# Performance work log

Measured on AMD Instinct MI355X. Metric: run time of the kernel, lower is better.

## Reference

```python
import jax, jax.numpy as jnp
import numpy as np

N, TX, NH, H, E, V = 64, 1024, 512, 512, 300, 32000
IP = NH + H            # attention input size = 1024
HALF = IP // 2         # 512
BN_EPS = 1e-5


def setup_inputs() -> dict:
    key = jax.random.key(0)
    ks = jax.random.split(key, 24)
    p = lambda k, shape: jax.random.normal(k, shape, dtype=jnp.float32) * 0.05
    embed_W = p(ks[0], (V, E)).at[0].set(0.0)  # padding_idx=0 row zeroed
    return {
        "yt_prev": jax.random.randint(ks[1], (N,), 0, V, dtype=jnp.int32),
        "h0": jax.random.normal(ks[2], (N, H), dtype=jnp.float32),
        "c0": jax.random.normal(ks[3], (N, H), dtype=jnp.float32),
        "h1": jax.random.normal(ks[4], (N, H), dtype=jnp.float32),
        "c1": jax.random.normal(ks[5], (N, H), dtype=jnp.float32),
        "encoder_output": jax.random.normal(ks[6], (N, TX, NH), dtype=jnp.float32),
        "c_prev": jax.random.normal(ks[7], (N, NH), dtype=jnp.float32),
        "embed_W": embed_W,
        # pre LSTM cell: input = NH + E
        "pre_W_ih": p(ks[8], (4 * H, NH + E)), "pre_W_hh": p(ks[9], (4 * H, H)),
        "pre_b_ih": p(ks[10], (4 * H,)), "pre_b_hh": p(ks[11], (4 * H,)),
        # post LSTM cell: input = H + NH
        "post_W_ih": p(ks[12], (4 * H, H + NH)), "post_W_hh": p(ks[13], (4 * H, H)),
        "post_b_ih": p(ks[14], (4 * H,)), "post_b_hh": p(ks[15], (4 * H,)),
        # attention MLP
        "att_W1": p(ks[16], (HALF, IP)), "att_b1": p(ks[17], (HALF,)),
        "att_W2": p(ks[18], (1, HALF)), "att_b2": p(ks[19], (1,)),
        # classifier
        "mlp_W": p(ks[20], (V, H)), "mlp_b": p(ks[21], (V,)),
        "bn_gamma": jnp.ones((V,), jnp.float32), "bn_beta": jnp.zeros((V,), jnp.float32),
    }


def _lstm_cell(x, h, c, W_ih, W_hh, b_ih, b_hh):
    # PyTorch LSTMCell gate order: i, f, g, o
    g = x @ W_ih.T + h @ W_hh.T + (b_ih + b_hh)
    i, f, gg, o = jnp.split(g, 4, axis=-1)
    c_new = jax.nn.sigmoid(f) * c + jax.nn.sigmoid(i) * jnp.tanh(gg)
    h_new = jax.nn.sigmoid(o) * jnp.tanh(c_new)
    return h_new, c_new


def reference(yt_prev, h0, c0, h1, c1, encoder_output, c_prev, embed_W,
              pre_W_ih, pre_W_hh, pre_b_ih, pre_b_hh,
              post_W_ih, post_W_hh, post_b_ih, post_b_hh,
              att_W1, att_b1, att_W2, att_b2,
              mlp_W, mlp_b, bn_gamma, bn_beta):
    # embedding lookup + concat with previous context
    y_emb = embed_W[yt_prev]                              # [N, E]
    rnn_input = jnp.concatenate([y_emb, c_prev], axis=1)  # [N, E+NH]
    h_0, c_0 = _lstm_cell(rnn_input, h0, c0, pre_W_ih, pre_W_hh, pre_b_ih, pre_b_hh)
    s_i = h_0
    # Bahdanau attention over encoder timesteps
    Tx = encoder_output.shape[1]
    s_exp = jnp.broadcast_to(s_i[:, None, :], (s_i.shape[0], Tx, s_i.shape[1]))
    concat = jnp.concatenate([encoder_output, s_exp], axis=2)  # [N, Tx, IP]
    e = jax.nn.relu(concat @ att_W1.T + att_b1)                # [N, Tx, HALF]
    scores = e @ att_W2.T + att_b2                             # [N, Tx, 1]
    alphas = jax.nn.softmax(scores, axis=1)                    # softmax over Tx
    context = jnp.sum(alphas * encoder_output, axis=1)         # [N, NH]
    # post LSTM cell
    spell_input = jnp.concatenate([s_i, context], axis=1)
    h_1, c_1 = _lstm_cell(spell_input, h1, c1, post_W_ih, post_W_hh, post_b_ih, post_b_hh)
    # classifier: linear -> relu -> batchnorm(train mode, batch stats) -> softmax
    z = jax.nn.relu(h_1 @ mlp_W.T + mlp_b)                     # [N, V]
    mean = jnp.mean(z, axis=0)
    var = jnp.mean((z - mean) ** 2, axis=0)                    # biased, as in PyTorch training
    z_bn = bn_gamma * (z - mean) * jax.lax.rsqrt(var + BN_EPS) + bn_beta
    out = jax.nn.softmax(z_bn, axis=1)
    return out, h_0, c_0, h_1, c_1, context
```

## Files before the change

### kernel.cpp

```cpp
#include <hip/hip_runtime.h>
#include <math.h>

#define DEVFN __device__ __forceinline__

typedef __attribute__((ext_vector_type(4))) float f32x4;
typedef __attribute__((ext_vector_type(8))) __bf16 bf16x8;
typedef __attribute__((ext_vector_type(4))) short short4v;
typedef __attribute__((ext_vector_type(8))) short short8v;

#define NB   64
#define TXD  1024
#define NHD  512
#define HSZ  512
#define ESZ  300
#define VSZ  32000
#define G4   (4*HSZ)
#define KPRE (ESZ + NHD + HSZ)
#define KPOST 1536
#define HALFD 512

DEVFN short f2bf(float f) {
  unsigned u = __float_as_uint(f);
  u = (u + 0x7fffu + ((u >> 16) & 1u)) >> 16;
  return (short)u;
}
DEVFN float sigm(float x) { return 1.0f / (1.0f + __expf(-x)); }

DEVFN short8v pack8(float4 a, float4 b) {
  short8v v;
  v[0]=f2bf(a.x); v[1]=f2bf(a.y); v[2]=f2bf(a.z); v[3]=f2bf(a.w);
  v[4]=f2bf(b.x); v[5]=f2bf(b.y); v[6]=f2bf(b.z); v[7]=f2bf(b.w);
  return v;
}
DEVFN short4v pack4(float4 a) {
  short4v v;
  v[0]=f2bf(a.x); v[1]=f2bf(a.y); v[2]=f2bf(a.z); v[3]=f2bf(a.w);
  return v;
}
DEVFN void gload16(const void* g, void* lds_base) {
  __builtin_amdgcn_global_load_lds(
      (const __attribute__((address_space(1))) unsigned int*)g,
      (__attribute__((address_space(3))) unsigned int*)lds_base, 16, 0, 0);
}

DEVFN float4 ldA4(const float* __restrict__ A, int lda, int row, int k, int Ka) {
  if (k >= Ka) { float4 z = {0.f,0.f,0.f,0.f}; return z; }
  return *(const float4*)(A + (size_t)row * lda + k);
}
DEVFN float4 ldB4(const float* __restrict__ B1, int ldb1, int split,
                  const float* __restrict__ B2, int ldb2, int row, int k, int Ka) {
  if (k >= Ka) { float4 z = {0.f,0.f,0.f,0.f}; return z; }
  if (k < split) return *(const float4*)(B1 + (size_t)row * ldb1 + k);
  return *(const float4*)(B2 + (size_t)row * ldb2 + (k - split));
}

__global__ __launch_bounds__(256)
void prep(const int* __restrict__ yt, const float* __restrict__ embW,
          const float* __restrict__ c_prev, const float* __restrict__ h0,
          const float* __restrict__ W1, unsigned short* __restrict__ W1b,
          float* __restrict__ cat)
{
  int b = blockIdx.x;
  if (b < 128) {
    int i = b * 256 + threadIdx.x;
    int c = i >> 6, kq = (i & 63) * 8;
    float4 a = *(const float4*)(W1 + (size_t)c * 1024 + kq);
    float4 bb = *(const float4*)(W1 + (size_t)c * 1024 + kq + 4);
    *(short8v*)(W1b + (size_t)c * 512 + kq) = pack8(a, bb);
  } else {
    int i = (b - 128) * 256 + threadIdx.x;
    if (i >= NB * KPRE) return;
    int n = i / KPRE, c = i - n * KPRE;
    float v;
    if (c < ESZ)            v = embW[(size_t)yt[n] * ESZ + c];
    else if (c < ESZ + NHD) v = c_prev[(size_t)n * NHD + (c - ESZ)];
    else                    v = h0[(size_t)n * HSZ + (c - ESZ - NHD)];
    cat[i] = v;
  }
}

template<int EPI>
__global__ __launch_bounds__(256)
void mfma_gemm128(const float* __restrict__ A, int lda, int Ka,
                  const float* __restrict__ B1, int ldb1, int split,
                  const float* __restrict__ B2, int ldb2,
                  const float* __restrict__ bias1,
                  float* __restrict__ C, int ldc, int Kslice,
                  const float* __restrict__ gamma, const float* __restrict__ beta,
                  float* __restrict__ bnsc, float* __restrict__ bnsh)
{
  __shared__ __align__(16) short As[64][40];
  __shared__ __align__(16) short Bs[128][40];
  const int tid = threadIdx.x;
  const int w = tid >> 6, lane = tid & 63;
  const int wr = w >> 1, wc = w & 1;
  const int cl = lane & 15, g = lane >> 4;
  const int n0 = blockIdx.x * 128;
  const int ks = blockIdx.y;
  const int kbeg = ks * Kslice;
  const int kend = min(kbeg + Kslice, Ka);
  C += (size_t)ks * 64 * ldc;

  const f32x4 fz = {0.f,0.f,0.f,0.f};
  f32x4 acc[2][4];
  #pragma unroll
  for (int i = 0; i < 2; ++i)
    #pragma unroll
    for (int j = 0; j < 4; ++j) acc[i][j] = fz;

  const int sr  = tid >> 2;
  const int skc = (tid & 3) * 8;

  float4 ra0, ra1, rb0[2], rb1[2];
  ra0 = ldA4(A, lda, sr, kbeg + skc, Ka);
  ra1 = ldA4(A, lda, sr, kbeg + skc + 4, Ka);
  #pragma unroll
  for (int it = 0; it < 2; ++it) {
    rb0[it] = ldB4(B1, ldb1, split, B2, ldb2, n0 + sr + it*64, kbeg + skc, Ka);
    rb1[it] = ldB4(B1, ldb1, split, B2, ldb2, n0 + sr + it*64, kbeg + skc + 4, Ka);
  }

  for (int k0 = kbeg; k0 < kend; k0 += 32) {
    __syncthreads();
    *(short8v*)&As[sr][skc] = pack8(ra0, ra1);
    #pragma unroll
    for (int it = 0; it < 2; ++it)
      *(short8v*)&Bs[sr + it*64][skc] = pack8(rb0[it], rb1[it]);
    __syncthreads();
    if (k0 + 32 < kend) {
      ra0 = ldA4(A, lda, sr, k0 + 32 + skc, Ka);
      ra1 = ldA4(A, lda, sr, k0 + 32 + skc + 4, Ka);
      #pragma unroll
      for (int it = 0; it < 2; ++it) {
        rb0[it] = ldB4(B1, ldb1, split, B2, ldb2, n0 + sr + it*64, k0 + 32 + skc, Ka);
        rb1[it] = ldB4(B1, ldb1, split, B2, ldb2, n0 + sr + it*64, k0 + 32 + skc + 4, Ka);
      }
    }
    bf16x8 af[2], bfr[4];
    #pragma unroll
    for (int mi = 0; mi < 2; ++mi)
      af[mi] = *(const bf16x8*)&As[wr*32 + mi*16 + cl][g * 8];
    #pragma unroll
    for (int ni = 0; ni < 4; ++ni)
      bfr[ni] = *(const bf16x8*)&Bs[wc*64 + ni*16 + cl][g * 8];
    #pragma unroll
    for (int mi = 0; mi < 2; ++mi)
      #pragma unroll
      for (int ni = 0; ni < 4; ++ni)
        acc[mi][ni] = __builtin_amdgcn_mfma_f32_16x16x32_bf16(af[mi], bfr[ni], acc[mi][ni], 0, 0, 0);
  }

  float s1[4] = {0.f,0.f,0.f,0.f}, s2[4] = {0.f,0.f,0.f,0.f};
  #pragma unroll
  for (int ni = 0; ni < 4; ++ni) {
    int nn = n0 + wc*64 + ni*16 + cl;
    float b = (EPI == 4) ? bias1[nn] : 0.f;
    #pragma unroll
    for (int mi = 0; mi < 2; ++mi)
      #pragma unroll
      for (int r = 0; r < 4; ++r) {
        int m = wr*32 + mi*16 + g*4 + r;
        float v = acc[mi][ni][r];
        if (EPI == 4) v = fmaxf(v + b, 0.f);
        C[(size_t)m * ldc + nn] = v;
        if (EPI == 4) { s1[ni] += v; s2[ni] = fmaf(v, v, s2[ni]); }
      }
  }
  if (EPI == 4) {
    #pragma unroll
    for (int mm = 16; mm < 64; mm <<= 1)
      #pragma unroll
      for (int ni = 0; ni < 4; ++ni) {
        s1[ni] += __shfl_xor(s1[ni], mm, 64);
        s2[ni] += __shfl_xor(s2[ni], mm, 64);
      }
    float* red = (float*)As;
    __syncthreads();
    if (g == 0) {
      #pragma unroll
      for (int ni = 0; ni < 4; ++ni) {
        int col = wc*64 + ni*16 + cl;
        red[(wr*128 + col)*2 + 0] = s1[ni];
        red[(wr*128 + col)*2 + 1] = s2[ni];
      }
    }
    __syncthreads();
    if (tid < 128) {
      int col = n0 + tid;
      float a1 = red[tid*2] + red[(128 + tid)*2];
      float a2 = red[tid*2 + 1] + red[(128 + tid)*2 + 1];
      float mean = a1 * (1.0f / NB);
      float var = a2 * (1.0f / NB) - mean * mean;
      float rr = rsqrtf(var + 1e-5f);
      float sc = gamma[col] * rr;
      bnsc[col] = sc;
      bnsh[col] = beta[col] - mean * sc;
    }
  }
}

__global__ __launch_bounds__(256)
void lstm_point2(const float* __restrict__ gp, int np,
                 const float* __restrict__ bih, const float* __restrict__ bhh,
                 const float* __restrict__ c_old,
                 float* __restrict__ h_new, float* __restrict__ c_new)
{
  int i = blockIdx.x * 256 + threadIdx.x;
  int n = i >> 9, k = i & 511;
  float g[4];
  #pragma unroll
  for (int j = 0; j < 4; ++j) {
    int idx = j * 512 + k;
    float s = bih[idx] + bhh[idx];
    for (int ks = 0; ks < np; ++ks)
      s += gp[((size_t)ks*64 + n) * G4 + idx];
    g[j] = s;
  }
  float c = sigm(g[1]) * c_old[i] + sigm(g[0]) * tanhf(g[2]);
  float h = sigm(g[3]) * tanhf(c);
  h_new[i] = h; c_new[i] = c;
}

__global__ __launch_bounds__(512)
void att_fused(const float* __restrict__ enc, const unsigned short* __restrict__ W1b,
               const float* __restrict__ W2, const float* __restrict__ sprojp,
               const float* __restrict__ b1,
               float* __restrict__ mbuf, float* __restrict__ sbuf,
               float* __restrict__ ctxp)
{
  __shared__ __align__(16) char Asmem[2 * 4096];
  __shared__ float red[512];
  __shared__ float eV[64];
  __shared__ __align__(16) f32x4 red4[512];
  const int tid = threadIdx.x;
  const int wid = tid >> 6, lane = tid & 63;
  const int cl = lane & 15, g = lane >> 4;
  const int r0 = blockIdx.x << 6;
  const int n  = blockIdx.x >> 4;
  const int c0 = wid << 6;

  const int a_row = tid >> 3, a_q = tid & 7;
  const int a_waddr = (a_row >> 1)*128 + (a_row & 1)*64
                    + (((a_q >> 1) ^ ((a_row >> 1) & 3)) << 4) + (a_q & 1)*8;
  const float* a_src = enc + (size_t)(r0 + a_row) * 512 + a_q * 4;
  const unsigned short* bp0 = W1b + (size_t)(c0 + cl) * 512 + g * 8;

  const f32x4 fz = {0.f,0.f,0.f,0.f};
  f32x4 acc[4][4];
  #pragma unroll
  for (int mi = 0; mi < 4; ++mi)
    #pragma unroll
    for (int ni = 0; ni < 4; ++ni) acc[mi][ni] = fz;

  float4 av;
  bf16x8 bcur[4], bnext[4];
  av = *(const float4*)(a_src);
  #pragma unroll
  for (int ni = 0; ni < 4; ++ni)
    bcur[ni] = *(const bf16x8*)(bp0 + ni * 8192);
  *(short4v*)(Asmem + a_waddr) = pack4(av);
  av = *(const float4*)(a_src + 32);
  asm volatile("s_waitcnt lgkmcnt(0)" ::: "memory");
  __builtin_amdgcn_s_barrier();
  __builtin_amdgcn_sched_barrier(0);

  for (int t = 0; t < 16; ++t) {
    const int s = t & 1;
    if (t < 15) {
      *(short4v*)(Asmem + (s ^ 1) * 4096 + a_waddr) = pack4(av);
      #pragma unroll
      for (int ni = 0; ni < 4; ++ni)
        bnext[ni] = *(const bf16x8*)(bp0 + ni * 8192 + (t + 1) * 32);
    }
    if (t < 14) av = *(const float4*)(a_src + (t + 2) * 32);
    const char* Ab = Asmem + s * 4096;
    bf16x8 af[4];
    #pragma unroll
    for (int mi = 0; mi < 4; ++mi) {
      int r = mi * 16 + cl;
      af[mi] = *(const bf16x8*)(Ab + (r >> 1) * 128 + (r & 1) * 64
                                + ((g ^ ((r >> 1) & 3)) << 4));
    }
    #pragma unroll
    for (int mi = 0; mi < 4; ++mi)
      #pragma unroll
      for (int ni = 0; ni < 4; ++ni)
        acc[mi][ni] = __builtin_amdgcn_mfma_f32_16x16x32_bf16(af[mi], bcur[ni], acc[mi][ni], 0, 0, 0);
    if (t < 15) {
      #pragma unroll
      for (int ni = 0; ni < 4; ++ni) bcur[ni] = bnext[ni];
      asm volatile("s_waitcnt lgkmcnt(0)" ::: "memory");
      __builtin_amdgcn_s_barrier();
      __builtin_amdgcn_sched_barrier(0);
    }
  }
  __syncthreads();

  float part[4][4] = {};
  #pragma unroll
  for (int ni = 0; ni < 4; ++ni) {
    int c = c0 + ni*16 + cl;
    float spv = b1[c];
    #pragma unroll
    for (int ks = 0; ks < 4; ++ks)
      spv += sprojp[((size_t)ks*64 + n) * HALFD + c];
    float w2 = W2[c];
    #pragma unroll
    for (int mi = 0; mi < 4; ++mi)
      #pragma unroll
      for (int r = 0; r < 4; ++r)
        part[mi][r] += fmaxf(acc[mi][ni][r] + spv, 0.f) * w2;
  }
  #pragma unroll
  for (int mm = 1; mm < 16; mm <<= 1)
    #pragma unroll
    for (int mi = 0; mi < 4; ++mi)
      #pragma unroll
      for (int r = 0; r < 4; ++r)
        part[mi][r] += __shfl_xor(part[mi][r], mm, 64);
  if (cl == 0) {
    #pragma unroll
    for (int mi = 0; mi < 4; ++mi)
      #pragma unroll
      for (int r = 0; r < 4; ++r)
        red[wid*64 + mi*16 + g*4 + r] = part[mi][r];
  }
  __syncthreads();
  if (tid < 64) {
    float s = 0.f;
    #pragma unroll
    for (int w = 0; w < 8; ++w) s += red[w*64 + tid];
    float M = s;
    #pragma unroll
    for (int mm = 32; mm >= 1; mm >>= 1) M = fmaxf(M, __shfl_xor(M, mm, 64));
    float e = __expf(s - M);
    eV[tid] = e;
    float S = e;
    #pragma unroll
    for (int mm = 32; mm >= 1; mm >>= 1) S += __shfl_xor(S, mm, 64);
    if (tid == 0) { mbuf[blockIdx.x] = M; sbuf[blockIdx.x] = S; }
  }
  __syncthreads();

  {
    const int cgrp = tid & 127, tq = tid >> 7;
    const float* ebase = enc + (size_t)r0 * 512 + (cgrp << 2);
    f32x4 a4 = fz;
    #pragma unroll 8
    for (int tt = 0; tt < 16; ++tt) {
      int t = tq*16 + tt;
      float et = eV[t];
      float4 x = *(const float4*)(ebase + (size_t)t * 512);
      a4[0] = fmaf(et, x.x, a4[0]);
      a4[1] = fmaf(et, x.y, a4[1]);
      a4[2] = fmaf(et, x.z, a4[2]);
      a4[3] = fmaf(et, x.w, a4[3]);
    }
    red4[tq*128 + cgrp] = a4;
  }
  __syncthreads();
  if (tid < 128) {
    f32x4 s4 = red4[tid];
    f32x4 b4 = red4[128 + tid];
    f32x4 c4 = red4[256 + tid];
    f32x4 d4 = red4[384 + tid];
    f32x4 o4;
    #pragma unroll
    for (int i = 0; i < 4; ++i) o4[i] = s4[i] + b4[i] + c4[i] + d4[i];
    *(f32x4*)(ctxp + (size_t)blockIdx.x * 512 + tid*4) = o4;
  }
}

__global__ __launch_bounds__(256)
void att_combine(const float* __restrict__ mbuf, const float* __restrict__ sbuf,
                 const float* __restrict__ ctxp, const float* __restrict__ h0out,
                 const float* __restrict__ h1in,
                 float* __restrict__ ctx_out, float* __restrict__ cat)
{
  int i = blockIdx.x * 256 + threadIdx.x;
  int n = i >> 9, c = i & 511;
  float M = -1e30f;
  #pragma unroll
  for (int b = 0; b < 16; ++b) M = fmaxf(M, mbuf[n*16 + b]);
  float S = 0.f, ctx = 0.f;
  #pragma unroll
  for (int b = 0; b < 16; ++b) {
    float w = __expf(mbuf[n*16 + b] - M);
    S = fmaf(sbuf[n*16 + b], w, S);
    ctx = fmaf(ctxp[(size_t)(n*16 + b)*512 + c], w, ctx);
  }
  ctx /= S;
  ctx_out[i] = ctx;
  cat[(size_t)n * KPOST + c] = h0out[i];
  cat[(size_t)n * KPOST + HSZ + c] = ctx;
  cat[(size_t)n * KPOST + 2*HSZ + c] = h1in[i];
}

__global__ __launch_bounds__(1024)
void softmax_v(const float* __restrict__ z, const float* __restrict__ scale,
               const float* __restrict__ shift, float* __restrict__ out)
{
  int n = blockIdx.x, tid = threadIdx.x;
  const float* zr = z + (size_t)n * VSZ;
  float* orow = out + (size_t)n * VSZ;
  __shared__ float rb[16];
  __shared__ float sb[16];
  float v[32]; float mx = -1e30f;
  #pragma unroll
  for (int i = 0; i < 32; ++i) {
    int j = tid + i*1024;
    v[i] = (j < VSZ) ? fmaf(zr[j], scale[j], shift[j]) : -1e30f;
    mx = fmaxf(mx, v[i]);
  }
  #pragma unroll
  for (int m = 32; m >= 1; m >>= 1) mx = fmaxf(mx, __shfl_xor(mx, m, 64));
  if ((tid & 63) == 0) rb[tid >> 6] = mx;
  __syncthreads();
  #pragma unroll
  for (int i = 0; i < 16; ++i) mx = fmaxf(mx, rb[i]);
  float s = 0.f;
  #pragma unroll
  for (int i = 0; i < 32; ++i) { v[i] = __expf(v[i] - mx); s += v[i]; }
  #pragma unroll
  for (int m = 32; m >= 1; m >>= 1) s += __shfl_xor(s, m, 64);
  if ((tid & 63) == 0) sb[tid >> 6] = s;
  __syncthreads();
  s = 0.f;
  #pragma unroll
  for (int i = 0; i < 16; ++i) s += sb[i];
  float inv = 1.0f / s;
  #pragma unroll
  for (int i = 0; i < 32; ++i) {
    int j = tid + i*1024;
    if (j < VSZ) orow[j] = v[i] * inv;
  }
}

extern "C" void kernel_launch(void* const* d_in, const int* in_sizes, int n_in,
                              void* d_out, int out_size, void* d_ws, size_t ws_size,
                              hipStream_t stream)
{
  const int*   yt       = (const int*)  d_in[0];
  const float* h0       = (const float*)d_in[1];
  const float* c0       = (const float*)d_in[2];
  const float* h1       = (const float*)d_in[3];
  const float* c1       = (const float*)d_in[4];
  const float* enc      = (const float*)d_in[5];
  const float* c_prev   = (const float*)d_in[6];
  const float* embW     = (const float*)d_in[7];
  const float* pre_Wih  = (const float*)d_in[8];
  const float* pre_Whh  = (const float*)d_in[9];
  const float* pre_bih  = (const float*)d_in[10];
  const float* pre_bhh  = (const float*)d_in[11];
  const float* post_Wih = (const float*)d_in[12];
  const float* post_Whh = (const float*)d_in[13];
  const float* post_bih = (const float*)d_in[14];
  const float* post_bhh = (const float*)d_in[15];
  const float* att_W1   = (const float*)d_in[16];
  const float* att_b1   = (const float*)d_in[17];
  const float* att_W2   = (const float*)d_in[18];
  const float* mlp_W    = (const float*)d_in[20];
  const float* mlp_b    = (const float*)d_in[21];
  const float* bn_g     = (const float*)d_in[22];
  const float* bn_b     = (const float*)d_in[23];

  float* out   = (float*)d_out;
  float* o_h0  = out + (size_t)NB * VSZ;
  float* o_c0  = o_h0 + NB * HSZ;
  float* o_h1  = o_c0 + NB * HSZ;
  float* o_c1  = o_h1 + NB * HSZ;
  float* o_ctx = o_c1 + NB * HSZ;

  float* ws = (float*)d_ws;
  float* pre_cat  = ws;
  float* gatesp   = ws + 84736;
  float* sprojp   = ws + 1264384;
  float* mbuf     = ws + 1395456;
  float* sbuf     = ws + 1396480;
  float* ctxp     = ws + 1397504;
  float* post_cat = ws + 1921792;
  unsigned short* W1b = (unsigned short*)(ws + 2020096);
  float* zbuf     = ws;
  float* bnsc     = ws + 2151168;
  float* bnsh     = ws + 2183168;

  prep<<<459, 256, 0, stream>>>(yt, embW, c_prev, h0, att_W1, W1b, pre_cat);
  mfma_gemm128<0><<<dim3(G4/128, 9), 256, 0, stream>>>(
      pre_cat, KPRE, KPRE, pre_Wih, ESZ + NHD, ESZ + NHD, pre_Whh, HSZ,
      nullptr, gatesp, G4, 160, nullptr, nullptr, nullptr, nullptr);
  lstm_point2<<<NB*HSZ/256, 256, 0, stream>>>(gatesp, 9, pre_bih, pre_bhh, c0, o_h0, o_c0);
  mfma_gemm128<0><<<dim3(HALFD/128, 4), 256, 0, stream>>>(
      o_h0, HSZ, HSZ, att_W1 + NHD, NHD + HSZ, HSZ, att_W1 + NHD, NHD + HSZ,
      nullptr, sprojp, HALFD, 128, nullptr, nullptr, nullptr, nullptr);
  att_fused<<<1024, 512, 0, stream>>>(enc, W1b, att_W2, sprojp, att_b1,
                                      mbuf, sbuf, ctxp);
  att_combine<<<NB*NHD/256, 256, 0, stream>>>(mbuf, sbuf, ctxp, o_h0, h1, o_ctx, post_cat);
  mfma_gemm128<0><<<dim3(G4/128, 8), 256, 0, stream>>>(
      post_cat, KPOST, KPOST, post_Wih, HSZ + NHD, HSZ + NHD, post_Whh, HSZ,
      nullptr, gatesp, G4, 192, nullptr, nullptr, nullptr, nullptr);
  lstm_point2<<<NB*HSZ/256, 256, 0, stream>>>(gatesp, 8, post_bih, post_bhh, c1, o_h1, o_c1);
  mfma_gemm128<4><<<dim3(VSZ/128, 1), 256, 0, stream>>>(
      o_h1, HSZ, HSZ, mlp_W, HSZ, HSZ, mlp_W, HSZ, mlp_b, zbuf, VSZ, 512,
      bn_g, bn_b, bnsc, bnsh);
  softmax_v<<<NB, 1024, 0, stream>>>(zbuf, bnsc, bnsh, out);
}
```

Baseline: 163.0 us.

## Preload full A tile to LDS in attention; split vocab softmax across blocks

In att_fused, the whole 64x512 encoder tile is converted to bf16 and held in a 128KB LDS buffer up front. The W1 tiles are then streamed into double-buffered LDS with global_load_lds, instead of each wave pulling its B fragments from global memory into registers. The vocab softmax is split into a partial max/sum kernel and a final normalize kernel over 4x64 blocks, replacing the 64 single-row blocks to raise parallelism. The cost is one extra launch, a second read of z, and a 128KB LDS footprint that allows only one block per CU.

After: 182.9 us. 1.12x slower.

```diff
diff --git a/kernel.cpp b/kernel.cpp
--- a/kernel.cpp
+++ b/kernel.cpp
@@ -5,7 +5,6 @@
 
 typedef __attribute__((ext_vector_type(4))) float f32x4;
 typedef __attribute__((ext_vector_type(8))) __bf16 bf16x8;
-typedef __attribute__((ext_vector_type(4))) short short4v;
 typedef __attribute__((ext_vector_type(8))) short short8v;
 
 #define NB   64
@@ -30,11 +29,6 @@
   short8v v;
   v[0]=f2bf(a.x); v[1]=f2bf(a.y); v[2]=f2bf(a.z); v[3]=f2bf(a.w);
   v[4]=f2bf(b.x); v[5]=f2bf(b.y); v[6]=f2bf(b.z); v[7]=f2bf(b.w);
-  return v;
-}
-DEVFN short4v pack4(float4 a) {
-  short4v v;
-  v[0]=f2bf(a.x); v[1]=f2bf(a.y); v[2]=f2bf(a.z); v[3]=f2bf(a.w);
   return v;
 }
 DEVFN void gload16(const void* g, void* lds_base) {
@@ -228,10 +222,7 @@
                float* __restrict__ mbuf, float* __restrict__ sbuf,
                float* __restrict__ ctxp)
 {
-  __shared__ __align__(16) char Asmem[2 * 4096];
-  __shared__ float red[512];
-  __shared__ float eV[64];
-  __shared__ __align__(16) f32x4 red4[512];
+  __shared__ __align__(16) char smem[131072];
   const int tid = threadIdx.x;
   const int wid = tid >> 6, lane = tid & 63;
   const int cl = lane & 15, g = lane >> 4;
@@ -239,11 +230,8 @@
   const int n  = blockIdx.x >> 4;
   const int c0 = wid << 6;
 
-  const int a_row = tid >> 3, a_q = tid & 7;
-  const int a_waddr = (a_row >> 1)*128 + (a_row & 1)*64
-                    + (((a_q >> 1) ^ ((a_row >> 1) & 3)) << 4) + (a_q & 1)*8;
-  const float* a_src = enc + (size_t)(r0 + a_row) * 512 + a_q * 4;
-  const unsigned short* bp0 = W1b + (size_t)(c0 + cl) * 512 + g * 8;
+  const int b_r = ((lane >> 3) << 1) + ((lane >> 2) & 1);
+  const int b_q = (((lane & 3) ^ ((lane >> 3) & 3)) << 3);
 
   const f32x4 fz = {0.f,0.f,0.f,0.f};
   f32x4 acc[4][4];
@@ -252,14 +240,27 @@
     #pragma unroll
     for (int ni = 0; ni < 4; ++ni) acc[mi][ni] = fz;
 
-  float4 av;
-  bf16x8 bcur[4], bnext[4];
-  av = *(const float4*)(a_src);
-  #pragma unroll
-  for (int ni = 0; ni < 4; ++ni)
-    bcur[ni] = *(const bf16x8*)(bp0 + ni * 8192);
-  *(short4v*)(Asmem + a_waddr) = pack4(av);
-  av = *(const float4*)(a_src + 32);
+  #define STAGE_B(buf, tt) do { int k0 = (tt) * 32; \
+    _Pragma("unroll") \
+    for (int jj = 0; jj < 4; ++jj) { \
+      int row = (wid << 6) + (jj << 4) + b_r; \
+      gload16(W1b + (size_t)row * 512 + k0 + b_q, \
+              smem + 65536 + (buf) * 32768 + (wid << 12) + (jj << 10)); } } while (0)
+
+  {
+    const int arow = tid >> 3, acb = (tid & 7) << 6;
+    const float* src = enc + (size_t)(r0 + arow) * 512 + acb;
+    float4 v[16];
+    #pragma unroll
+    for (int i = 0; i < 16; ++i) v[i] = *(const float4*)(src + i*4);
+    #pragma unroll
+    for (int j = 0; j < 8; ++j) {
+      int s = ((tid & 7) << 3) + j;
+      *(short8v*)(smem + arow*1024 + ((s ^ (arow & 7)) << 4)) = pack8(v[2*j], v[2*j+1]);
+    }
+  }
+  STAGE_B(0, 0);
+  asm volatile("s_waitcnt vmcnt(0)" ::: "memory");
   asm volatile("s_waitcnt lgkmcnt(0)" ::: "memory");
   __builtin_amdgcn_s_barrier();
   __builtin_amdgcn_sched_barrier(0);
@@ -267,33 +268,33 @@
   for (int t = 0; t < 16; ++t) {
     const int s = t & 1;
     if (t < 15) {
-      *(short4v*)(Asmem + (s ^ 1) * 4096 + a_waddr) = pack4(av);
-      #pragma unroll
-      for (int ni = 0; ni < 4; ++ni)
-        bnext[ni] = *(const bf16x8*)(bp0 + ni * 8192 + (t + 1) * 32);
-    }
-    if (t < 14) av = *(const float4*)(a_src + (t + 2) * 32);
-    const char* Ab = Asmem + s * 4096;
+      STAGE_B(s ^ 1, t + 1);
+      __builtin_amdgcn_sched_barrier(0);
+    }
+    const char* Bb = smem + 65536 + s * 32768;
     bf16x8 af[4];
     #pragma unroll
     for (int mi = 0; mi < 4; ++mi) {
       int r = mi * 16 + cl;
-      af[mi] = *(const bf16x8*)(Ab + (r >> 1) * 128 + (r & 1) * 64
-                                + ((g ^ ((r >> 1) & 3)) << 4));
-    }
-    #pragma unroll
-    for (int mi = 0; mi < 4; ++mi)
-      #pragma unroll
-      for (int ni = 0; ni < 4; ++ni)
-        acc[mi][ni] = __builtin_amdgcn_mfma_f32_16x16x32_bf16(af[mi], bcur[ni], acc[mi][ni], 0, 0, 0);
+      af[mi] = *(const bf16x8*)(smem + r * 1024 + ((((t<<2)+g) ^ (r & 7)) << 4));
+    }
+    #pragma unroll
+    for (int ni = 0; ni < 4; ++ni) {
+      int r = wid * 64 + ni * 16 + cl;
+      bf16x8 bf = *(const bf16x8*)(Bb + (r >> 1 & 255) * 128 - (wid<<13) + (wid<<13)
+                                   + ((r & 1) << 6) + ((g ^ ((r >> 1) & 3)) << 4));
+      #pragma unroll
+      for (int mi = 0; mi < 4; ++mi)
+        acc[mi][ni] = __builtin_amdgcn_mfma_f32_16x16x32_bf16(af[mi], bf, acc[mi][ni], 0, 0, 0);
+    }
     if (t < 15) {
-      #pragma unroll
-      for (int ni = 0; ni < 4; ++ni) bcur[ni] = bnext[ni];
+      asm volatile("s_waitcnt vmcnt(0)" ::: "memory");
       asm volatile("s_waitcnt lgkmcnt(0)" ::: "memory");
       __builtin_amdgcn_s_barrier();
       __builtin_amdgcn_sched_barrier(0);
     }
   }
+  #undef STAGE_B
   __syncthreads();
 
   float part[4][4] = {};
@@ -318,6 +319,8 @@
       #pragma unroll
       for (int r = 0; r < 4; ++r)
         part[mi][r] += __shfl_xor(part[mi][r], mm, 64);
+  float* red = (float*)smem;
+  float* eV  = (float*)(smem + 2048);
   if (cl == 0) {
     #pragma unroll
     for (int mi = 0; mi < 4; ++mi)
@@ -342,6 +345,7 @@
   }
   __syncthreads();
 
+  f32x4* red4 = (f32x4*)(smem + 65536);
   {
     const int cgrp = tid & 127, tq = tid >> 7;
     const float* ebase = enc + (size_t)r0 * 512 + (cgrp << 2);
@@ -396,43 +400,65 @@
   cat[(size_t)n * KPOST + 2*HSZ + c] = h1in[i];
 }
 
-__global__ __launch_bounds__(1024)
-void softmax_v(const float* __restrict__ z, const float* __restrict__ scale,
-               const float* __restrict__ shift, float* __restrict__ out)
-{
-  int n = blockIdx.x, tid = threadIdx.x;
+__global__ __launch_bounds__(256)
+void smv_part(const float* __restrict__ z, const float* __restrict__ scale,
+              const float* __restrict__ shift,
+              float* __restrict__ pm, float* __restrict__ ps)
+{
+  int vq = blockIdx.x, n = blockIdx.y, tid = threadIdx.x;
+  int base = vq * 8000;
   const float* zr = z + (size_t)n * VSZ;
-  float* orow = out + (size_t)n * VSZ;
-  __shared__ float rb[16];
-  __shared__ float sb[16];
+  __shared__ float rb[4], sb[4];
   float v[32]; float mx = -1e30f;
   #pragma unroll
   for (int i = 0; i < 32; ++i) {
-    int j = tid + i*1024;
-    v[i] = (j < VSZ) ? fmaf(zr[j], scale[j], shift[j]) : -1e30f;
+    int o = tid + i*256;
+    int j = base + o;
+    v[i] = (o < 8000) ? fmaf(zr[j], scale[j], shift[j]) : -1e30f;
     mx = fmaxf(mx, v[i]);
   }
   #pragma unroll
   for (int m = 32; m >= 1; m >>= 1) mx = fmaxf(mx, __shfl_xor(mx, m, 64));
   if ((tid & 63) == 0) rb[tid >> 6] = mx;
   __syncthreads();
-  #pragma unroll
-  for (int i = 0; i < 16; ++i) mx = fmaxf(mx, rb[i]);
+  mx = fmaxf(fmaxf(rb[0], rb[1]), fmaxf(rb[2], rb[3]));
   float s = 0.f;
   #pragma unroll
-  for (int i = 0; i < 32; ++i) { v[i] = __expf(v[i] - mx); s += v[i]; }
+  for (int i = 0; i < 32; ++i) {
+    int o = tid + i*256;
+    if (o < 8000) s += __expf(v[i] - mx);
+  }
   #pragma unroll
   for (int m = 32; m >= 1; m >>= 1) s += __shfl_xor(s, m, 64);
   if ((tid & 63) == 0) sb[tid >> 6] = s;
   __syncthreads();
-  s = 0.f;
-  #pragma unroll
-  for (int i = 0; i < 16; ++i) s += sb[i];
-  float inv = 1.0f / s;
+  if (tid == 0) {
+    pm[n*4 + vq] = mx;
+    ps[n*4 + vq] = sb[0] + sb[1] + sb[2] + sb[3];
+  }
+}
+
+__global__ __launch_bounds__(256)
+void smv_final(const float* __restrict__ z, const float* __restrict__ scale,
+               const float* __restrict__ shift,
+               const float* __restrict__ pm, const float* __restrict__ ps,
+               float* __restrict__ out)
+{
+  int vq = blockIdx.x, n = blockIdx.y, tid = threadIdx.x;
+  int base = vq * 8000;
+  const float* zr = z + (size_t)n * VSZ;
+  float M = fmaxf(fmaxf(pm[n*4], pm[n*4+1]), fmaxf(pm[n*4+2], pm[n*4+3]));
+  float S = 0.f;
+  #pragma unroll
+  for (int k = 0; k < 4; ++k) S = fmaf(ps[n*4+k], __expf(pm[n*4+k] - M), S);
+  float inv = 1.0f / S;
   #pragma unroll
   for (int i = 0; i < 32; ++i) {
-    int j = tid + i*1024;
-    if (j < VSZ) orow[j] = v[i] * inv;
+    int o = tid + i*256;
+    if (o < 8000) {
+      int j = base + o;
+      out[(size_t)n * VSZ + j] = __expf(fmaf(zr[j], scale[j], shift[j]) - M) * inv;
+    }
   }
 }
 
@@ -483,6 +509,8 @@
   float* zbuf     = ws;
   float* bnsc     = ws + 2151168;
   float* bnsh     = ws + 2183168;
+  float* pm       = ws + 2215168;
+  float* psb      = ws + 2215424;
 
   prep<<<459, 256, 0, stream>>>(yt, embW, c_prev, h0, att_W1, W1b, pre_cat);
   mfma_gemm128<0><<<dim3(G4/128, 9), 256, 0, stream>>>(
@@ -502,5 +530,6 @@
   mfma_gemm128<4><<<dim3(VSZ/128, 1), 256, 0, stream>>>(
       o_h1, HSZ, HSZ, mlp_W, HSZ, HSZ, mlp_W, HSZ, mlp_b, zbuf, VSZ, 512,
       bn_g, bn_b, bnsc, bnsh);
-  softmax_v<<<NB, 1024, 0, stream>>>(zbuf, bnsc, bnsh, out);
-}
+  smv_part<<<dim3(4, NB), 256, 0, stream>>>(zbuf, bnsc, bnsh, pm, psb);
+  smv_final<<<dim3(4, NB), 256, 0, stream>>>(zbuf, bnsc, bnsh, pm, psb, out);
+}
```

## Stage attention W1 tiles into LDS via direct global-to-LDS loads

Applied to the files above, without the earlier changes.

The attention GEMM kernel stops loading W1 bf16 fragments straight into registers. It now stages them into a double-buffered, swizzled LDS region using gload16 direct global-to-LDS transfers, and the waits switch to vmcnt counters. All shared arrays are merged into one 72KB buffer that is reused for the reductions afterwards. This cuts register pressure and the uncoalesced per-lane B loads, but the larger LDS footprint may lower occupancy.

After: 151.3 us. 7.2% less time.

```diff
diff --git a/kernel.cpp b/kernel.cpp
--- a/kernel.cpp
+++ b/kernel.cpp
@@ -228,10 +228,7 @@
                float* __restrict__ mbuf, float* __restrict__ sbuf,
                float* __restrict__ ctxp)
 {
-  __shared__ __align__(16) char Asmem[2 * 4096];
-  __shared__ float red[512];
-  __shared__ float eV[64];
-  __shared__ __align__(16) f32x4 red4[512];
+  __shared__ __align__(16) char smem[73728];
   const int tid = threadIdx.x;
   const int wid = tid >> 6, lane = tid & 63;
   const int cl = lane & 15, g = lane >> 4;
@@ -240,10 +237,12 @@
   const int c0 = wid << 6;
 
   const int a_row = tid >> 3, a_q = tid & 7;
-  const int a_waddr = (a_row >> 1)*128 + (a_row & 1)*64
-                    + (((a_q >> 1) ^ ((a_row >> 1) & 3)) << 4) + (a_q & 1)*8;
   const float* a_src = enc + (size_t)(r0 + a_row) * 512 + a_q * 4;
-  const unsigned short* bp0 = W1b + (size_t)(c0 + cl) * 512 + g * 8;
+  const int a_line = a_row >> 1;
+  const int a_waddr = a_line*128 + (a_row & 1)*64
+                    + (((a_q >> 1) ^ (a_line & 3)) << 4) + (a_q & 1)*8;
+  const int b_r = ((lane >> 3) << 1) + ((lane >> 2) & 1);
+  const int b_q = (((lane & 3) ^ ((lane >> 3) & 3)) << 3);
 
   const f32x4 fz = {0.f,0.f,0.f,0.f};
   f32x4 acc[4][4];
@@ -253,13 +252,24 @@
     for (int ni = 0; ni < 4; ++ni) acc[mi][ni] = fz;
 
   float4 av;
-  bf16x8 bcur[4], bnext[4];
-  av = *(const float4*)(a_src);
-  #pragma unroll
-  for (int ni = 0; ni < 4; ++ni)
-    bcur[ni] = *(const bf16x8*)(bp0 + ni * 8192);
-  *(short4v*)(Asmem + a_waddr) = pack4(av);
-  av = *(const float4*)(a_src + 32);
+  #define A_LOAD(tt)  (av = *(const float4*)(a_src + (tt) * 32))
+  #define A_WRITE(buf) (*(short4v*)(smem + (buf) * 4096 + a_waddr) = pack4(av))
+  #define STAGE_B(buf, tt) do { int k0 = (tt) * 32; \
+    _Pragma("unroll") \
+    for (int jj = 0; jj < 4; ++jj) { \
+      int row = (wid << 6) + (jj << 4) + b_r; \
+      gload16(W1b + (size_t)row * 512 + k0 + b_q, \
+              smem + 8192 + (buf) * 32768 + (wid << 12) + (jj << 10)); } } while (0)
+
+  A_LOAD(0);
+  __builtin_amdgcn_sched_barrier(0);
+  asm volatile("s_waitcnt vmcnt(0)" ::: "memory");
+  A_WRITE(0);
+  STAGE_B(0, 0);
+  __builtin_amdgcn_sched_barrier(0);
+  A_LOAD(1);
+  __builtin_amdgcn_sched_barrier(0);
+  asm volatile("s_waitcnt vmcnt(1)" ::: "memory");
   asm volatile("s_waitcnt lgkmcnt(0)" ::: "memory");
   __builtin_amdgcn_s_barrier();
   __builtin_amdgcn_sched_barrier(0);
@@ -267,13 +277,17 @@
   for (int t = 0; t < 16; ++t) {
     const int s = t & 1;
     if (t < 15) {
-      *(short4v*)(Asmem + (s ^ 1) * 4096 + a_waddr) = pack4(av);
-      #pragma unroll
-      for (int ni = 0; ni < 4; ++ni)
-        bnext[ni] = *(const bf16x8*)(bp0 + ni * 8192 + (t + 1) * 32);
-    }
-    if (t < 14) av = *(const float4*)(a_src + (t + 2) * 32);
-    const char* Ab = Asmem + s * 4096;
+      asm volatile("s_waitcnt vmcnt(0)" ::: "memory");
+      A_WRITE(s ^ 1);
+      STAGE_B(s ^ 1, t + 1);
+      __builtin_amdgcn_sched_barrier(0);
+      if (t < 14) {
+        A_LOAD(t + 2);
+        __builtin_amdgcn_sched_barrier(0);
+      }
+    }
+    const char* Ab = smem + s * 4096;
+    const char* Bb = smem + 8192 + s * 32768;
     bf16x8 af[4];
     #pragma unroll
     for (int mi = 0; mi < 4; ++mi) {
@@ -282,18 +296,25 @@
                                 + ((g ^ ((r >> 1) & 3)) << 4));
     }
     #pragma unroll
-    for (int mi = 0; mi < 4; ++mi)
-      #pragma unroll
-      for (int ni = 0; ni < 4; ++ni)
-        acc[mi][ni] = __builtin_amdgcn_mfma_f32_16x16x32_bf16(af[mi], bcur[ni], acc[mi][ni], 0, 0, 0);
+    for (int ni = 0; ni < 4; ++ni) {
+      int r = wid * 64 + ni * 16 + cl;
+      bf16x8 bf = *(const bf16x8*)(Bb + (r >> 1) * 128 + (r & 1) * 64
+                                   + ((g ^ ((r >> 1) & 3)) << 4));
+      #pragma unroll
+      for (int mi = 0; mi < 4; ++mi)
+        acc[mi][ni] = __builtin_amdgcn_mfma_f32_16x16x32_bf16(af[mi], bf, acc[mi][ni], 0, 0, 0);
+    }
     if (t < 15) {
-      #pragma unroll
-      for (int ni = 0; ni < 4; ++ni) bcur[ni] = bnext[ni];
+      if (t < 14) asm volatile("s_waitcnt vmcnt(1)" ::: "memory");
+      else        asm volatile("s_waitcnt vmcnt(0)" ::: "memory");
       asm volatile("s_waitcnt lgkmcnt(0)" ::: "memory");
       __builtin_amdgcn_s_barrier();
       __builtin_amdgcn_sched_barrier(0);
     }
   }
+  #undef A_LOAD
+  #undef A_WRITE
+  #undef STAGE_B
   __syncthreads();
 
   float part[4][4] = {};
@@ -318,6 +339,8 @@
       #pragma unroll
       for (int r = 0; r < 4; ++r)
         part[mi][r] += __shfl_xor(part[mi][r], mm, 64);
+  float* red = (float*)smem;
+  float* eV  = (float*)(smem + 2048);
   if (cl == 0) {
     #pragma unroll
     for (int mi = 0; mi < 4; ++mi)
@@ -342,6 +365,7 @@
   }
   __syncthreads();
 
+  f32x4* red4 = (f32x4*)(smem + 8192);
   {
     const int cgrp = tid & 127, tq = tid >> 7;
     const float* ebase = enc + (size_t)r0 * 512 + (cgrp << 2);
```
